# Kernel tuning notes

Hardware: AMD Instinct MI355X
Metric: run time of the kernel (lower is better)

## Reference

```python
import jax, jax.numpy as jnp
import numpy as np

B, N, V, K = 2, 4096, 32768, 128
BLUR = 0.05  # geomloss blur; eps = blur**p with p=2
# geomloss 'multiscale' eps-annealing: sigma from ~diameter down to blur with scaling=0.5,
# then a few extra iterations at the final eps.
SIGMAS = [2.0, 1.0, 0.5, 0.25, 0.125, 0.0625, BLUR]
EPS_LIST = [s * s for s in SIGMAS] + [BLUR * BLUR] * 5


def setup_inputs() -> dict:
    key = jax.random.key(0)
    k1, k2, k3, k4 = jax.random.split(key, 4)
    y_hat = jax.random.uniform(k1, (B, 3, V), dtype=jnp.float32)          # voxel densities
    xyz = jax.random.uniform(k2, (B, N, 3), dtype=jnp.float32)            # point positions
    w = jax.random.uniform(k3, (B, N, 3), dtype=jnp.float32)              # fx, fy, fz weights
    y = jnp.concatenate([xyz, w], axis=-1)                                # [B, N, 6]
    voxel_centers = jax.random.uniform(k4, (V, 3), dtype=jnp.float32)
    return {"y_hat": y_hat, "y": y, "voxel_centers": voxel_centers}


def _sqdist(x, y):
    # x: [B,n,3], y: [B,m,3] -> [B,n,m]
    xn = jnp.sum(x * x, axis=-1)
    yn = jnp.sum(y * y, axis=-1)
    d = xn[..., :, None] + yn[..., None, :] - 2.0 * jnp.einsum('bnd,bmd->bnm', x, y)
    return jnp.maximum(d, 0.0)


def _softmin(eps, C, h):
    # C: [B,n,m], h: [B,m] -> -eps * logsumexp_j(h_j - C_ij/eps): [B,n]
    return -eps * jax.nn.logsumexp(h[:, None, :] - C / eps, axis=-1)


def _loop_ab(a_log, b_log, C):
    # symmetric (averaged) Sinkhorn updates with eps annealing
    Ct = jnp.swapaxes(C, -1, -2)
    f = jnp.zeros(a_log.shape, C.dtype)
    g = jnp.zeros(b_log.shape, C.dtype)
    for eps in EPS_LIST:
        ft = _softmin(eps, C, b_log + g / eps)
        gt = _softmin(eps, Ct, a_log + f / eps)
        f, g = 0.5 * (f + ft), 0.5 * (g + gt)
    return f, g


def _loop_sym(a_log, C):
    # self-correlation (debiasing) potential: f = g by symmetry
    f = jnp.zeros(a_log.shape, C.dtype)
    for eps in EPS_LIST:
        f = 0.5 * (f + _softmin(eps, C, a_log + f / eps))
    return f


def _sinkhorn_div(a, x, b, y_pts, C_xx):
    # debiased Sinkhorn divergence S_eps(a,x ; b,y), p=2 cost C = |x-y|^2 / 2
    eps = EPS_LIST[-1]
    a_log = jnp.log(jnp.maximum(a, 1e-20))
    b_log = jnp.log(jnp.maximum(b, 1e-20))
    C_xy = 0.5 * _sqdist(x, y_pts)        # [B,N,K]
    C_yy = 0.5 * _sqdist(y_pts, y_pts)    # [B,K,K]
    # run annealed iterations without grad (geomloss envelope-theorem style),
    # then one final differentiable update
    f0, g0 = jax.lax.stop_gradient(_loop_ab(a_log, b_log, C_xy))
    fa0 = jax.lax.stop_gradient(_loop_sym(a_log, C_xx))
    gb0 = jax.lax.stop_gradient(_loop_sym(b_log, C_yy))
    F_ab = _softmin(eps, C_xy, b_log + g0 / eps)
    G_ab = _softmin(eps, jnp.swapaxes(C_xy, -1, -2), a_log + f0 / eps)
    F_a = _softmin(eps, C_xx, a_log + fa0 / eps)
    G_b = _softmin(eps, C_yy, b_log + gb0 / eps)
    return jnp.sum(a * (F_ab - F_a), axis=-1) + jnp.sum(b * (G_ab - G_b), axis=-1)


def reference(y_hat, y, voxel_centers):
    xyz = y[:, :, :3]                                   # [B,N,3]
    yh = y_hat.reshape(y_hat.shape[0], y_hat.shape[1], -1)  # [B,3,V]
    C_xx = 0.5 * _sqdist(xyz, xyz)                      # [B,N,N] shared self-cost
    total = jnp.zeros((), xyz.dtype)
    for c in range(3):
        w = y[:, :, 3 + c]                              # [B,N] weights (fx/fy/fz)
        vals, idx = jax.lax.top_k(yh[:, c], K)          # [B,K] top-K voxel densities
        pts = voxel_centers[idx]                        # [B,K,3] gathered centers
        total = total + jnp.sum(_sinkhorn_div(w, xyz, vals, pts, C_xx))
    return total
```

## Files before the change

kernel.cpp:

```cpp
#include <hip/hip_runtime.h>
#include <math.h>

#define B_   2
#define N_   4096
#define V_   32768
#define K_   128
#define SC   16
#define CH   3
#define NEPS 12
#define XXB  512
#define FTB  96
#define GTB  192
#define YYB  6
#define NBLK (XXB + FTB + GTB + YYB)
#define TCAP 2048

#define LOG2E 1.4426950408889634f
#define LN2   0.6931471805599453f
#define EPS_LAST 0.0025f

typedef float f2 __attribute__((ext_vector_type(2)));

__device__ __forceinline__ float fexp2(float x) {
  float r; asm("v_exp_f32 %0, %1" : "=v"(r) : "v"(x)); return r;
}
__device__ __forceinline__ float flog2(float x) {
  float r; asm("v_log_f32 %0, %1" : "=v"(r) : "v"(x)); return r;
}

__device__ float4 g_P   [B_*N_];
__device__ float  g_alog[B_*CH*N_];
__device__ float  g_fa  [2][B_*CH*N_];
__device__ float  g_partS[2][SC*CH*B_*N_];
__device__ float  g_Ubar[2][B_*SC*CH];
__device__ float4 g_pts [B_*CH*K_];
__device__ float  g_blog[B_*CH*K_];
__device__ float  g_bval[B_*CH*K_];
__device__ float  g_fbuf[2][B_*CH*N_];
__device__ float  g_gbuf[2][B_*CH*K_];
__device__ float  g_ybuf[2][B_*CH*K_];
__device__ float  g_S1a[FTB];
__device__ float  g_Gab[768];
__device__ float  g_S2[6];
__device__ float  g_S3[96];

__device__ __forceinline__ void lse_up(float t, float& m, float& s) {
  float mn = fmaxf(m, t);
  float e  = fexp2(-fabsf(t - m));
  bool  gt = t > m;
  float mulv = gt ? e : 1.0f;
  float addv = gt ? 1.0f : e;
  s = fmaf(s, mulv, addv);
  m = mn;
}
__device__ __forceinline__ void lse_merge(float& M, float& S, float oM, float oS) {
  float mn = fmaxf(M, oM);
  float e  = fexp2(-fabsf(M - oM));
  bool  gt = oM > M;
  float sm = gt ? e : 1.0f;
  float so = gt ? 1.0f : e;
  S = fmaf(S, sm, oS * so);
  M = mn;
}

__global__ __launch_bounds__(1024) void k_prep(const float* __restrict__ y) {
  const int bn = blockIdx.x * 1024 + threadIdx.x;
  const int b = bn >> 12, n = bn & (N_ - 1);
  const float* yr = y + (size_t)bn * 6;
  float x0 = yr[0], x1 = yr[1], x2 = yr[2];
  g_P[bn] = make_float4(x0, x1, x2, 0.5f * (x0*x0 + x1*x1 + x2*x2));
#pragma unroll
  for (int c = 0; c < CH; ++c) {
    float w  = yr[3 + c];
    float al = flog2(fmaxf(w, 1e-20f)) * LN2;
    const int o = (b*CH + c)*N_ + n;
    g_alog[o] = al; g_fa[0][o] = 0.f; g_fbuf[0][o] = 0.f;
  }
}

__global__ __launch_bounds__(1024) void k_topk(const float* __restrict__ yhat,
                                               const float* __restrict__ vox) {
  const int bc = blockIdx.x, tid = threadIdx.x;
  __shared__ int   s_hist[8192];
  __shared__ int   s_suf[1024];
  __shared__ float s_tv[TCAP];
  __shared__ int   s_ti[TCAP];
  __shared__ float s_wv[K_];
  __shared__ int   s_wi[K_];
  __shared__ int   s_wtot[16];
  __shared__ int   s_pos, s_eq, s_bs, s_c1, s_cnt;

  if (tid < K_) { g_gbuf[0][bc*K_ + tid] = 0.f; g_ybuf[0][bc*K_ + tid] = 0.f; }
#pragma unroll
  for (int j = 0; j < 8; ++j) s_hist[tid + j*1024] = 0;
  if (tid == 0) { s_pos = 0; s_eq = 0; }

  const float* row = yhat + (size_t)bc * V_;
  float v[32];
#pragma unroll
  for (int j = 0; j < 32; ++j) v[j] = row[tid + j * 1024];
  __syncthreads();
#pragma unroll
  for (int j = 0; j < 32; ++j) {
    unsigned b = __float_as_uint(v[j]);
    unsigned bk = (b >> 31) ? 0u : min(b >> 17, 8191u);
    atomicAdd(&s_hist[bk], 1);
  }
  __syncthreads();
  const int base = tid * 8;
  int cs = 0;
#pragma unroll
  for (int i = 0; i < 8; ++i) cs += s_hist[base + i];
  s_suf[tid] = cs;
  __syncthreads();
  for (int off = 1; off < 1024; off <<= 1) {
    int vv = s_suf[tid];
    int add = (tid + off < 1024) ? s_suf[tid + off] : 0;
    __syncthreads();
    s_suf[tid] = vv + add;
    __syncthreads();
  }
  int nxt = (tid < 1023) ? s_suf[tid + 1] : 0;
  if (s_suf[tid] >= K_ && nxt < K_) {
    int cnt = nxt, bstar = base, c1 = nxt;
    for (int b2 = base + 7; b2 >= base; --b2) {
      int h = s_hist[b2];
      if (cnt + h >= K_) { bstar = b2; c1 = cnt; break; }
      cnt += h;
    }
    s_bs = bstar; s_c1 = c1;
  }
  __syncthreads();
  const int bstar = s_bs, c1 = s_c1;
#pragma unroll
  for (int j = 0; j < 32; ++j) {
    unsigned b = __float_as_uint(v[j]);
    int bk = (b >> 31) ? 0 : (int)min(b >> 17, 8191u);
    int i = tid + j * 1024;
    if (bk > bstar) {
      int p = atomicAdd(&s_pos, 1);
      s_wv[p] = v[j]; s_wi[p] = i;
    } else if (bk == bstar) {
      int p = atomicAdd(&s_eq, 1);
      if (p < TCAP) { s_tv[p] = v[j]; s_ti[p] = i; }
    }
  }
  __syncthreads();
  const int tcnt = s_eq;
  if (tcnt <= TCAP) {
    const int need = K_ - c1;
    for (int e = tid; e < tcnt; e += 1024) {
      float vv = s_tv[e]; int i = s_ti[e];
      int rank = 0;
      for (int j2 = 0; j2 < tcnt; ++j2) {
        float ov = s_tv[j2]; int oi = s_ti[j2];
        rank += (ov > vv || (ov == vv && oi < i)) ? 1 : 0;
      }
      if (rank < need) { s_wv[c1 + rank] = vv; s_wi[c1 + rank] = i; }
    }
    __syncthreads();
  } else {
    unsigned lo = 0u, hi = 0x7f800000u;
    while (lo < hi) {
      unsigned mid = lo + ((hi - lo + 1u) >> 1);
      if (tid == 0) s_cnt = 0;
      __syncthreads();
      int local = 0;
#pragma unroll
      for (int j = 0; j < 32; ++j) local += (__float_as_uint(v[j]) >= mid) ? 1 : 0;
      for (int off = 32; off; off >>= 1) local += __shfl_down(local, off);
      if ((tid & 63) == 0 && local) atomicAdd(&s_cnt, local);
      __syncthreads();
      int cnt = s_cnt;
      __syncthreads();
      if (cnt >= K_) lo = mid; else hi = mid - 1u;
    }
    const unsigned T = lo;
    if (tid == 0) s_cnt = 0;
    __syncthreads();
#pragma unroll
    for (int j = 0; j < 32; ++j) {
      if (__float_as_uint(v[j]) > T) {
        int p = atomicAdd(&s_cnt, 1);
        s_wv[p] = v[j]; s_wi[p] = tid + j * 1024;
      }
    }
    __syncthreads();
    int got = s_cnt;
    __syncthreads();
    for (int chunk = 0; chunk < 32 && got < K_; ++chunk) {
      int i = chunk * 1024 + tid;
      bool f = (__float_as_uint(v[chunk]) == T);
      unsigned long long mask = __ballot(f);
      int lane = tid & 63, wv = tid >> 6;
      int wpre = __popcll(mask & ((1ULL << lane) - 1ULL));
      if (lane == 0) s_wtot[wv] = __popcll(mask);
      __syncthreads();
      int pre = wpre, tot = 0;
      for (int w = 0; w < 16; ++w) { if (w < wv) pre += s_wtot[w]; tot += s_wtot[w]; }
      if (f && got + pre < K_) { s_wv[got + pre] = v[chunk]; s_wi[got + pre] = i; }
      got = min(got + tot, K_);
      __syncthreads();
    }
  }
  if (tid < K_) {
    float mv = s_wv[tid]; int mi = s_wi[tid];
    float p0 = vox[(size_t)mi*3+0], p1 = vox[(size_t)mi*3+1], p2 = vox[(size_t)mi*3+2];
    g_pts [bc*K_ + tid] = make_float4(p0, p1, p2, 0.5f*(p0*p0 + p1*p1 + p2*p2));
    g_bval[bc*K_ + tid] = mv;
    g_blog[bc*K_ + tid] = flog2(fmaxf(mv, 1e-20f)) * LN2;
  }
}

__global__ __launch_bounds__(256) void k_pass(float eps, float eps_prev, int it, int mode,
                                              const float* __restrict__ y) {
  const float il = LOG2E / eps, nil = -il;
  const int blk = blockIdx.x, tid = threadIdx.x;
  const int src = it & 1;
  __shared__ float s_M[2048];
  __shared__ float s_scale[48];
  __shared__ float s_Mx[3];
  __shared__ float s_w[12];

  if (blk < XXB) {
    const int J = blk & 15;
    const int I = (blk >> 4) & 15;
    const int b = blk >> 8;
    const int r  = (J << 8) + tid;
    const int bn_r = b*N_ + r;
    float U[CH];
    if (it == 0) {
#pragma unroll
      for (int c = 0; c < CH; ++c) U[c] = LOG2E * g_alog[(b*CH + c)*N_ + r];
    } else {
      const int pv = src ^ 1;
      if (tid < 48) {
        int c = tid >> 4, Jp = tid & 15;
        s_scale[tid] = g_Ubar[pv][(b*SC + Jp)*CH + c];
      }
      __syncthreads();
      if (tid < 3) {
        float mm = s_scale[tid*16];
#pragma unroll
        for (int j = 1; j < 16; ++j) mm = fmaxf(mm, s_scale[tid*16 + j]);
        s_Mx[tid] = mm;
      }
      __syncthreads();
      if (tid < 48) s_scale[tid] = fexp2(s_scale[tid] - s_Mx[tid >> 4]);
      __syncthreads();
#pragma unroll
      for (int c = 0; c < CH; ++c) {
        float S = 0.f;
#pragma unroll
        for (int Jp = 0; Jp < 16; ++Jp)
          S = fmaf(g_partS[pv][(Jp*CH + c)*(B_*N_) + bn_r], s_scale[c*16 + Jp], S);
        float sm = -eps_prev * LN2 * (s_Mx[c] + flog2(S));
        const int o = (b*CH + c)*N_ + r;
        float fn = 0.5f * (g_fa[src ^ 1][o] + sm);
        g_fa[src][o] = fn;
        U[c] = fmaf(fn, il, LOG2E * g_alog[o]);
      }
      __syncthreads();
    }
    float Ub[CH];
#pragma unroll
    for (int c = 0; c < CH; ++c) {
      float u = U[c];
      for (int off = 32; off; off >>= 1) u = fmaxf(u, __shfl_xor(u, off));
      if ((tid & 63) == 0) s_w[(tid >> 6)*3 + c] = u;
    }
    __syncthreads();
#pragma unroll
    for (int c = 0; c < CH; ++c)
      Ub[c] = fmaxf(fmaxf(s_w[c], s_w[3 + c]), fmaxf(s_w[6 + c], s_w[9 + c]));
    if (tid < 3) g_Ubar[src][(b*SC + J)*CH + tid] = Ub[tid];
    {
      float4 Pm = g_P[bn_r];
      const int pp = tid >> 1, par = tid & 1;
      float* rec = s_M + pp*16;
      rec[0 + par] = il * Pm.x;
      rec[2 + par] = il * Pm.y;
      rec[4 + par] = il * Pm.z;
      rec[6 + par] = -il * Pm.w;
#pragma unroll
      for (int c = 0; c < CH; ++c) rec[8 + 2*c + par] = fexp2(U[c] - Ub[c]);
    }
    __syncthreads();
    const int bn0 = b*N_ + (I << 8) + tid;
    const float4 Pn0 = g_P[bn0];
    const float xs0 = Pn0.x, ys0 = Pn0.y, zs0 = Pn0.z, nn0 = nil * Pn0.w;
    const f2 zz = {0.f, 0.f};
    f2 a00 = zz, a01 = zz, a02 = zz;
#pragma unroll 4
    for (int j = 0; j < 128; ++j) {
      const float* Mj = s_M + j*16;
      const float4 q0 = *(const float4*)(Mj);
      const float4 q1 = *(const float4*)(Mj + 4);
      const float4 q2 = *(const float4*)(Mj + 8);
      const float2 q3 = *(const float2*)(Mj + 12);
      f2 t0 = f2{q1.z, q1.w} + nn0;
      t0 = f2{q1.x, q1.y} * zs0 + t0;
      t0 = f2{q0.z, q0.w} * ys0 + t0;
      t0 = f2{q0.x, q0.y} * xs0 + t0;
      t0 = __builtin_elementwise_min(t0, zz);
      f2 e0; e0.x = fexp2(t0.x); e0.y = fexp2(t0.y);
      a00 = f2{q2.x, q2.y} * e0 + a00;
      a01 = f2{q2.z, q2.w} * e0 + a01;
      a02 = f2{q3.x, q3.y} * e0 + a02;
    }
    float* pc = g_partS[src];
    pc[(J*CH + 0)*(B_*N_) + bn0] = a00.x + a00.y;
    pc[(J*CH + 1)*(B_*N_) + bn0] = a01.x + a01.y;
    pc[(J*CH + 2)*(B_*N_) + bn0] = a02.x + a02.y;
  } else if (blk < XXB + FTB) {
    float4* s_A = (float4*)s_M;
    float*  s_C = s_M + 512;
    float*  s_D = s_M + 640;
    const int blk2 = blk - XXB;
    const int bc = blk2 >> 4;
    const int b = bc / 3, c = bc % 3;
    const int n = ((blk2 & 15) << 8) + tid;
    float Hk = -INFINITY;
    if (tid < K_) {
      float g = g_gbuf[src][bc*K_ + tid];
      Hk = fmaf(g, il, LOG2E * g_blog[bc*K_ + tid]);
      s_A[tid] = g_pts[bc*K_ + tid];
    }
    float hm = Hk;
    for (int off = 32; off; off >>= 1) hm = fmaxf(hm, __shfl_xor(hm, off));
    if ((tid & 63) == 0) s_w[tid >> 6] = hm;
    __syncthreads();
    const float Hbar = fmaxf(fmaxf(s_w[0], s_w[1]), fmaxf(s_w[2], s_w[3]));
    if (tid < K_) { float dh = Hk - Hbar; s_C[tid] = fexp2(dh); s_D[tid] = dh; }
    float4 Pn = g_P[b*N_ + n];
    __syncthreads();
    float S = 0.f, T = 0.f, M = -INFINITY;
#pragma unroll 4
    for (int k2 = 0; k2 < K_; k2 += 2) {
      float4 p1 = s_A[k2];
      float d1 = fmaf(Pn.x, p1.x, fmaf(Pn.y, p1.y, Pn.z * p1.z));
      float C1 = fmaxf((Pn.w + p1.w) - d1, 0.f);
      float w1 = C1 * nil;
      S = fmaf(s_C[k2], fexp2(w1), S);
      M = fmaxf(M, w1 + s_D[k2]);
      float4 p2 = s_A[k2+1];
      float d2 = fmaf(Pn.x, p2.x, fmaf(Pn.y, p2.y, Pn.z * p2.z));
      float C2 = fmaxf((Pn.w + p2.w) - d2, 0.f);
      float w2 = C2 * nil;
      T = fmaf(s_C[k2+1], fexp2(w2), T);
      M = fmaxf(M, w2 + s_D[k2+1]);
    }
    S += T;
    float lse = (S > 0.f) ? flog2(S) : M;
    float ft = -eps * LN2 * (Hbar + lse);
    if (mode == 0) {
      g_fbuf[src ^ 1][bc*N_ + n] = 0.5f * (g_fbuf[src][bc*N_ + n] + ft);
    } else {
      float a = y[(size_t)(b*N_ + n) * 6 + 3 + c];
      float acc = a * ft;
      for (int off = 32; off; off >>= 1) acc += __shfl_down(acc, off);
      __syncthreads();
      if ((tid & 63) == 0) s_w[tid >> 6] = acc;
      __syncthreads();
      if (tid == 0) g_S1a[blk2] = s_w[0] + s_w[1] + s_w[2] + s_w[3];
    }
  } else if (blk < XXB + FTB + GTB) {
    const int job = (blk - (XXB + FTB)) * 4 + (tid >> 6);
    const int bc = job >> 7, k = job & (K_ - 1);
    const int b = bc / 3;
    const int lane = tid & 63;
    float4 Pk = g_pts[bc*K_ + k];
    float M0=-INFINITY,S0=0.f,M1=-INFINITY,S1=0.f,M2=-INFINITY,S2=0.f,M3=-INFINITY,S3=0.f;
    for (int j = 0; j < 64; j += 4) {
#pragma unroll
      for (int u = 0; u < 4; ++u) {
        int n = ((j + u) << 6) + lane;
        float4 pm = g_P[b*N_ + n];
        float Hn = fmaf(g_fbuf[src][bc*N_ + n], il, LOG2E * g_alog[bc*N_ + n]);
        float d = fmaf(Pk.x, pm.x, fmaf(Pk.y, pm.y, Pk.z * pm.z));
        float C = fmaxf((Pk.w + pm.w) - d, 0.f);
        float t = fmaf(C, nil, Hn);
        if (u == 0) lse_up(t, M0, S0);
        else if (u == 1) lse_up(t, M1, S1);
        else if (u == 2) lse_up(t, M2, S2);
        else lse_up(t, M3, S3);
      }
    }
    lse_merge(M0, S0, M1, S1);
    lse_merge(M2, S2, M3, S3);
    lse_merge(M0, S0, M2, S2);
    for (int off = 1; off < 64; off <<= 1) {
      float oM = __shfl_xor(M0, off);
      float oS = __shfl_xor(S0, off);
      lse_merge(M0, S0, oM, oS);
    }
    if (lane == 0) {
      float gt = -eps * LN2 * (M0 + flog2(S0));
      const int o = bc*K_ + k;
      if (mode == 0) g_gbuf[src ^ 1][o] = 0.5f * (g_gbuf[src][o] + gt);
      else           g_Gab[job] = g_bval[o] * gt;
    }
  } else {
    float4* s_A = (float4*)s_M;
    float*  s_C = s_M + 512;
    float*  s_D = s_M + 640;
    const int bc = blk - (XXB + FTB + GTB);
    const int k = tid & (K_ - 1);
    if (tid < K_) {
      s_A[tid] = g_pts[bc*K_ + tid];
      float g = g_ybuf[src][bc*K_ + tid];
      s_C[tid] = fmaf(g, il, LOG2E * g_blog[bc*K_ + tid]);
      s_D[tid] = g;
    }
    __syncthreads();
    float4 Pk = s_A[k];
    float M = -INFINITY, S = 0.f;
    for (int m = 0; m < K_; ++m) {
      float4 pm = s_A[m];
      float d = fmaf(Pk.x, pm.x, fmaf(Pk.y, pm.y, Pk.z * pm.z));
      float C = fmaxf((Pk.w + pm.w) - d, 0.f);
      lse_up(fmaf(C, nil, s_C[m]), M, S);
    }
    float sv = -eps * LN2 * (M + flog2(S));
    if (mode == 0) {
      if (tid < K_) g_ybuf[src ^ 1][bc*K_ + k] = 0.5f * (s_D[k] + sv);
    } else {
      float val = (tid < K_) ? g_bval[bc*K_ + k] * sv : 0.f;
      for (int off = 32; off; off >>= 1) val += __shfl_down(val, off);
      __syncthreads();
      if ((tid & 63) == 0) s_w[tid >> 6] = val;
      __syncthreads();
      if (tid == 0) g_S2[bc] = s_w[0] + s_w[1] + s_w[2] + s_w[3];
    }
  }
}

__global__ __launch_bounds__(256) void k_finalize(const float* __restrict__ y) {
  const int tid = threadIdx.x;
  const int idx = blockIdx.x * 256 + tid;
  const int c  = idx >> 13;
  const int bn = idx & (B_*N_ - 1);
  const int b = bn >> 12, n = bn & (N_ - 1);
  __shared__ float s_scale[SC];
  __shared__ float s_mm;
  __shared__ float s_w[4];
  if (tid < SC) s_scale[tid] = g_Ubar[0][(b*SC + tid)*CH + c];
  __syncthreads();
  if (tid == 0) {
    float mm = s_scale[0];
#pragma unroll
    for (int s = 1; s < SC; ++s) mm = fmaxf(mm, s_scale[s]);
    s_mm = mm;
  }
  __syncthreads();
  const float Mmax = s_mm;
  if (tid < SC) s_scale[tid] = fexp2(s_scale[tid] - Mmax);
  __syncthreads();
  float S = 0.f;
#pragma unroll
  for (int s = 0; s < SC; ++s)
    S = fmaf(g_partS[0][(s*CH + c)*(B_*N_) + bn], s_scale[s], S);
  float sm = -EPS_LAST * LN2 * (Mmax + flog2(S));
  float a = y[(size_t)(b*N_ + n)*6 + 3 + c];
  float acc = a * sm;
  for (int off = 32; off; off >>= 1) acc += __shfl_down(acc, off);
  if ((tid & 63) == 0) s_w[tid >> 6] = acc;
  __syncthreads();
  if (tid == 0) g_S3[blockIdx.x] = s_w[0] + s_w[1] + s_w[2] + s_w[3];
}

__global__ __launch_bounds__(1024) void k_total(float* __restrict__ out) {
  const int tid = threadIdx.x;
  float local = 0.f;
  if (tid < 768) local += g_Gab[tid];
  if (tid < FTB) local += g_S1a[tid];
  if (tid < 96)  local -= g_S3[tid];
  if (tid < 6)   local -= g_S2[tid];
  for (int off = 32; off; off >>= 1) local += __shfl_down(local, off);
  __shared__ float s_red[16];
  if ((tid & 63) == 0) s_red[tid >> 6] = local;
  __syncthreads();
  if (tid == 0) {
    float t = 0.f;
#pragma unroll
    for (int i = 0; i < 16; ++i) t += s_red[i];
    out[0] = t;
  }
}

extern "C" void kernel_launch(void* const* d_in, const int* in_sizes, int n_in,
                              void* d_out, int out_size, void* d_ws, size_t ws_size,
                              hipStream_t stream) {
  const float* y_hat = (const float*)d_in[0];
  const float* y     = (const float*)d_in[1];
  const float* vox   = (const float*)d_in[2];
  float* out = (float*)d_out;

  static const float eps_list[NEPS + 1] = {4.0f, 1.0f, 0.25f, 0.0625f, 0.015625f, 0.00390625f,
                                           0.0025f, 0.0025f, 0.0025f, 0.0025f, 0.0025f, 0.0025f,
                                           EPS_LAST};

  k_prep<<<8, 1024, 0, stream>>>(y);
  k_topk<<<6, 1024, 0, stream>>>(y_hat, vox);
  for (int it = 0; it <= NEPS; ++it) {
    float eps_prev = (it > 0) ? eps_list[it - 1] : 1.0f;
    int mode = (it == NEPS) ? 1 : 0;
    k_pass<<<NBLK, 256, 0, stream>>>(eps_list[it], eps_prev, it, mode, y);
  }
  k_finalize<<<96, 256, 0, stream>>>(y);
  k_total<<<1, 1024, 0, stream>>>(out);
}
```

Before: 261.6 us.

## Compute self-cost exponent tile with bf16 split-precision MFMA instead of scalar FMAs

The N×N self-cost softmin tile now builds its exponent argument with MFMA 16x16x32 bf16 instructions. Point coordinates are split into hi/lo bf16 pairs to recover near-fp32 accuracy. A precomputed A-operand image is written in k_prep, and the B operand is built per block in shared memory, with the squared-norm term folded in as the accumulator init. This moves the dominant per-pair FMA work onto matrix cores, leaving only the exp and the weighted accumulation on vector ALUs. It adds cross-lane shuffle reductions, and the hi/lo split may still lose accuracy at small eps.

```diff
diff --git a/kernel.cpp b/kernel.cpp
--- a/kernel.cpp
+++ b/kernel.cpp
@@ -19,7 +19,8 @@
 #define LN2   0.6931471805599453f
 #define EPS_LAST 0.0025f
 
-typedef float f2 __attribute__((ext_vector_type(2)));
+typedef float f32x4 __attribute__((ext_vector_type(4)));
+typedef short bf16x8 __attribute__((ext_vector_type(8)));
 
 __device__ __forceinline__ float fexp2(float x) {
   float r; asm("v_exp_f32 %0, %1" : "=v"(r) : "v"(x)); return r;
@@ -27,6 +28,11 @@
 __device__ __forceinline__ float flog2(float x) {
   float r; asm("v_log_f32 %0, %1" : "=v"(r) : "v"(x)); return r;
 }
+__device__ __forceinline__ ushort bfh(float f) {
+  unsigned u = __float_as_uint(f);
+  return (ushort)((u + 0x7FFFu + ((u >> 16) & 1u)) >> 16);
+}
+__device__ __forceinline__ float bff(ushort s) { return __uint_as_float(((unsigned)s) << 16); }
 
 __device__ float4 g_P   [B_*N_];
 __device__ float  g_alog[B_*CH*N_];
@@ -43,6 +49,7 @@
 __device__ float  g_Gab[768];
 __device__ float  g_S2[6];
 __device__ float  g_S3[96];
+__device__ short  g_Aimg[B_*256*64*8];
 
 __device__ __forceinline__ void lse_up(float t, float& m, float& s) {
   float mn = fmaxf(m, t);
@@ -76,6 +83,18 @@
     const int o = (b*CH + c)*N_ + n;
     g_alog[o] = al; g_fa[0][o] = 0.f; g_fbuf[0][o] = 0.f;
   }
+  ushort xh = bfh(x0), yh = bfh(x1), zh = bfh(x2);
+  ushort xl = bfh(x0 - bff(xh)), yl = bfh(x1 - bff(yh)), zl = bfh(x2 - bff(zh));
+  const ushort ONE = 0x3F80;
+  bf16x8 v0 = {(short)xh,(short)yh,(short)zh,(short)ONE,(short)xl,(short)yl,(short)zl,(short)ONE};
+  bf16x8 v1 = {(short)xh,(short)yh,(short)zh,0,0,0,0,0};
+  bf16x8 vz = {0,0,0,0,0,0,0,0};
+  bf16x8* img = (bf16x8*)g_Aimg;
+  const size_t base = (size_t)(b*256 + (n >> 4)) * 64 + (n & 15);
+  img[base]      = v0;
+  img[base + 16] = v1;
+  img[base + 32] = vz;
+  img[base + 48] = vz;
 }
 
 __global__ __launch_bounds__(1024) void k_topk(const float* __restrict__ yhat,
@@ -217,10 +236,13 @@
   const float il = LOG2E / eps, nil = -il;
   const int blk = blockIdx.x, tid = threadIdx.x;
   const int src = it & 1;
-  __shared__ float s_M[2048];
-  __shared__ float s_scale[48];
-  __shared__ float s_Mx[3];
-  __shared__ float s_w[12];
+  __shared__ bf16x8 s_B[1024];
+  __shared__ float  s_EU[1024];
+  __shared__ float  s_nn[256];
+  __shared__ float  s_scale[48];
+  __shared__ float  s_Mx[3];
+  __shared__ float  s_w[12];
+  float* s_M = (float*)s_B;
 
   if (blk < XXB) {
     const int J = blk & 15;
@@ -274,44 +296,86 @@
     for (int c = 0; c < CH; ++c)
       Ub[c] = fmaxf(fmaxf(s_w[c], s_w[3 + c]), fmaxf(s_w[6 + c], s_w[9 + c]));
     if (tid < 3) g_Ubar[src][(b*SC + J)*CH + tid] = Ub[tid];
-    {
-      float4 Pm = g_P[bn_r];
-      const int pp = tid >> 1, par = tid & 1;
-      float* rec = s_M + pp*16;
-      rec[0 + par] = il * Pm.x;
-      rec[2 + par] = il * Pm.y;
-      rec[4 + par] = il * Pm.z;
-      rec[6 + par] = -il * Pm.w;
-#pragma unroll
-      for (int c = 0; c < CH; ++c) rec[8 + 2*c + par] = fexp2(U[c] - Ub[c]);
-    }
-    __syncthreads();
-    const int bn0 = b*N_ + (I << 8) + tid;
-    const float4 Pn0 = g_P[bn0];
-    const float xs0 = Pn0.x, ys0 = Pn0.y, zs0 = Pn0.z, nn0 = nil * Pn0.w;
-    const f2 zz = {0.f, 0.f};
-    f2 a00 = zz, a01 = zz, a02 = zz;
-#pragma unroll 4
-    for (int j = 0; j < 128; ++j) {
-      const float* Mj = s_M + j*16;
-      const float4 q0 = *(const float4*)(Mj);
-      const float4 q1 = *(const float4*)(Mj + 4);
-      const float4 q2 = *(const float4*)(Mj + 8);
-      const float2 q3 = *(const float2*)(Mj + 12);
-      f2 t0 = f2{q1.z, q1.w} + nn0;
-      t0 = f2{q1.x, q1.y} * zs0 + t0;
-      t0 = f2{q0.z, q0.w} * ys0 + t0;
-      t0 = f2{q0.x, q0.y} * xs0 + t0;
-      t0 = __builtin_elementwise_min(t0, zz);
-      f2 e0; e0.x = fexp2(t0.x); e0.y = fexp2(t0.y);
-      a00 = f2{q2.x, q2.y} * e0 + a00;
-      a01 = f2{q2.z, q2.w} * e0 + a01;
-      a02 = f2{q3.x, q3.y} * e0 + a02;
-    }
-    float* pc = g_partS[src];
-    pc[(J*CH + 0)*(B_*N_) + bn0] = a00.x + a00.y;
-    pc[(J*CH + 1)*(B_*N_) + bn0] = a01.x + a01.y;
-    pc[(J*CH + 2)*(B_*N_) + bn0] = a02.x + a02.y;
+    s_EU[tid*4 + 0] = fexp2(U[0] - Ub[0]);
+    s_EU[tid*4 + 1] = fexp2(U[1] - Ub[1]);
+    s_EU[tid*4 + 2] = fexp2(U[2] - Ub[2]);
+    s_EU[tid*4 + 3] = 0.f;
+    s_nn[tid] = nil * g_P[b*N_ + (I << 8) + tid].w;
+#pragma unroll
+    for (int j = 0; j < 4; ++j) {
+      int img = tid + (j << 8);
+      int mt = img >> 6, l2 = img & 63, g = l2 >> 4, mm = (mt << 4) + (l2 & 15);
+      float4 Q = g_P[b*N_ + (J << 8) + mm];
+      float xt = il*Q.x, yt = il*Q.y, zt = il*Q.z, qt = nil*Q.w;
+      ushort xh = bfh(xt), yh = bfh(yt), zh = bfh(zt), qh = bfh(qt);
+      bf16x8 vv;
+      if (g == 0) {
+        ushort ql = bfh(qt - bff(qh));
+        vv = bf16x8{(short)xh,(short)yh,(short)zh,(short)qh,
+                    (short)xh,(short)yh,(short)zh,(short)ql};
+      } else if (g == 1) {
+        ushort xl = bfh(xt - bff(xh)), yl = bfh(yt - bff(yh)), zl = bfh(zt - bff(zh));
+        vv = bf16x8{(short)xl,(short)yl,(short)zl,0,0,0,0,0};
+      } else {
+        vv = bf16x8{0,0,0,0,0,0,0,0};
+      }
+      s_B[img] = vv;
+    }
+    __syncthreads();
+    const int w = tid >> 6, l = tid & 63;
+    bf16x8 A[4]; f32x4 nn4[4];
+#pragma unroll
+    for (int j = 0; j < 4; ++j) {
+      int nt = (w << 2) + j;
+      A[j] = ((const bf16x8*)g_Aimg)[(size_t)((b*256 + (I << 4) + nt)*64 + l)];
+      nn4[j] = *(const f32x4*)&s_nn[(nt << 4) + ((l >> 4) << 2)];
+    }
+    f32x4 S[4][3];
+#pragma unroll
+    for (int j = 0; j < 4; ++j)
+#pragma unroll
+      for (int c = 0; c < 3; ++c) S[j][c] = f32x4{0.f, 0.f, 0.f, 0.f};
+    for (int mt = 0; mt < 16; ++mt) {
+      bf16x8 Bf = s_B[(mt << 6) + l];
+      f32x4 eu = *(const f32x4*)&s_EU[((mt << 4) + (l & 15)) << 2];
+#pragma unroll
+      for (int j = 0; j < 4; ++j) {
+        f32x4 acc = __builtin_amdgcn_mfma_f32_16x16x32_bf16(A[j], Bf, nn4[j], 0, 0, 0);
+        f32x4 e;
+        e.x = fexp2(acc.x); e.y = fexp2(acc.y); e.z = fexp2(acc.z); e.w = fexp2(acc.w);
+        S[j][0] += eu.x * e;
+        S[j][1] += eu.y * e;
+        S[j][2] += eu.z * e;
+      }
+    }
+#pragma unroll
+    for (int j = 0; j < 4; ++j)
+#pragma unroll
+      for (int c = 0; c < 3; ++c) {
+        f32x4 v = S[j][c];
+#pragma unroll
+        for (int off = 1; off <= 8; off <<= 1) {
+          v.x += __shfl_xor(v.x, off);
+          v.y += __shfl_xor(v.y, off);
+          v.z += __shfl_xor(v.z, off);
+          v.w += __shfl_xor(v.w, off);
+        }
+        S[j][c] = v;
+      }
+    if ((l & 15) == 0) {
+      const int g = l >> 4;
+      float* pc = g_partS[src];
+#pragma unroll
+      for (int j = 0; j < 4; ++j) {
+        int n = (I << 8) + (((w << 2) + j) << 4) + (g << 2);
+#pragma unroll
+        for (int c = 0; c < 3; ++c) {
+          float* dst = pc + (size_t)(J*CH + c)*(B_*N_) + b*N_ + n;
+          dst[0] = S[j][c][0]; dst[1] = S[j][c][1];
+          dst[2] = S[j][c][2]; dst[3] = S[j][c][3];
+        }
+      }
+    }
   } else if (blk < XXB + FTB) {
     float4* s_A = (float4*)s_M;
     float*  s_C = s_M + 512;
```

New measurement: 305.8 us. 16.9% more time.
